# Kernel tuning notes

Hardware: AMD Instinct MI355X
Metric: run time of the kernel (lower is better)

The kernel has to match this reference:

```python
import jax, jax.numpy as jnp
import numpy as np

B, S, D, H = 2, 2048, 1024, 16
DH = D // H  # 64


def setup_inputs() -> dict:
    key = jax.random.key(0)
    ks = jax.random.split(key, 9)
    def rn(k, shape, scale=1.0):
        return jax.random.normal(k, shape, dtype=jnp.float32) * scale
    w_scale = 1.0 / np.sqrt(D)
    return {
        "queries": rn(ks[0], (B, S, D)),
        "keys": rn(ks[1], (B, S, D)),
        "values": rn(ks[2], (B, S, D)),
        "Wq": rn(ks[3], (D, D), w_scale),
        "bq": rn(ks[4], (D,), w_scale),
        "Wk": rn(ks[5], (D, D), w_scale),
        "bk": rn(ks[6], (D,), w_scale),
        "Wv": rn(ks[7], (D, D), w_scale),
        "bv": rn(ks[8], (D,), w_scale),
    }


def _split_heads(x):
    # torch: cat(split(x, DH, dim=-1), dim=0) -> index (h*B + b); equivalent to
    # [B,S,H,DH] -> [H,B,S,DH]
    bsz, slen, _ = x.shape
    return x.reshape(bsz, slen, H, DH).transpose(2, 0, 1, 3)


def reference(queries, keys, values, Wq, bq, Wk, bk, Wv, bv):
    # Linear projections (W stored so that y = x @ W + b)
    Q = queries @ Wq + bq
    K = keys @ Wk + bk
    V = values @ Wv + bv

    Qh = _split_heads(Q)  # [H,B,S,DH]
    Kh = _split_heads(K)
    Vh = _split_heads(V)

    scale = 1.0 / jnp.sqrt(jnp.asarray(DH, dtype=Qh.dtype))
    scores = jnp.einsum("hbqd,hbkd->hbqk", Qh, Kh) * scale  # [H,B,S,S]
    attn = jax.nn.softmax(scores, axis=-1)  # dropout_rate=0 -> identity
    out = jnp.einsum("hbqk,hbkd->hbqd", attn, Vh)  # [H,B,S,DH]

    # torch: cat(split(out, B, dim=0), dim=2) -> [B,S,H*DH] with head h in slice h
    out = out.transpose(1, 2, 0, 3).reshape(queries.shape[0], queries.shape[1], D)
    return out + queries  # residual; NOTE: W_O is defined but unused in the original forward
```

## Files before the change

### kernel.cpp

```cpp
#include <hip/hip_runtime.h>
#include <hip/hip_bf16.h>
#include <math.h>

#define BB 2
#define SS 2048
#define DD 1024
#define HH 16
#define DHH 64
#define MM (BB * SS)

typedef float f32x4 __attribute__((ext_vector_type(4)));
typedef __bf16 bf16x8 __attribute__((ext_vector_type(8)));

#define N_QKV ((size_t)MM * DD)
#define N_W   ((size_t)DD * DD)

__device__ unsigned short g_X [3][N_QKV];
__device__ unsigned short g_Q [N_QKV];
__device__ unsigned short g_K [N_QKV];
__device__ unsigned short g_Vt[N_QKV];
__device__ unsigned short g_Wt[3][N_W];

__device__ __forceinline__ unsigned short f2bu(float f) {
    unsigned u = __float_as_uint(f);
    unsigned r = u + 0x7FFFu + ((u >> 16) & 1u);
    return (unsigned short)(r >> 16);
}

union FragU { uint4 u; bf16x8 v; unsigned short s[8]; };
static __device__ __forceinline__ bf16x8 ldfrag(const unsigned short* p) {
    FragU f; f.u = *(const uint4*)p; return f.v;
}

__global__ __launch_bounds__(256) void cvt3(
        const float* __restrict__ x0, const float* __restrict__ x1,
        const float* __restrict__ x2, unsigned short* __restrict__ X)
{
    const float* src = blockIdx.y == 0 ? x0 : (blockIdx.y == 1 ? x1 : x2);
    unsigned short* dst = X + (size_t)blockIdx.y * N_QKV;
    const size_t i = ((size_t)blockIdx.x * 256 + threadIdx.x) * 4;
    const float4 v = *(const float4*)(src + i);
    ushort4 s;
    s.x = f2bu(v.x); s.y = f2bu(v.y); s.z = f2bu(v.z); s.w = f2bu(v.w);
    *(ushort4*)(dst + i) = s;
}

__global__ __launch_bounds__(256) void transpose_w3(
        const float* __restrict__ W0, const float* __restrict__ W1,
        const float* __restrict__ W2, unsigned short* __restrict__ Wt3)
{
    const float* W = blockIdx.z == 0 ? W0 : (blockIdx.z == 1 ? W1 : W2);
    unsigned short* Wt = Wt3 + (size_t)blockIdx.z * N_W;
    __shared__ float Ts[64][65];
    const int t = threadIdx.x;
    const int k0 = blockIdx.y * 64, n0 = blockIdx.x * 64;
#pragma unroll
    for (int i = 0; i < 16; ++i) {
        const int f = t + 256 * i, r = f >> 6, c = f & 63;
        Ts[r][c] = W[(size_t)(k0 + r) * DD + n0 + c];
    }
    __syncthreads();
#pragma unroll
    for (int i = 0; i < 16; ++i) {
        const int f = t + 256 * i, r = f >> 6, c = f & 63;
        Wt[(size_t)(n0 + r) * DD + k0 + c] = f2bu(Ts[c][r]);
    }
}

__global__ __launch_bounds__(256) void proj3(
        const unsigned short* __restrict__ X, const unsigned short* __restrict__ Wt3,
        const float* __restrict__ bq, const float* __restrict__ bk,
        const float* __restrict__ bv,
        unsigned short* __restrict__ Qp, unsigned short* __restrict__ Kp,
        unsigned short* __restrict__ Vtp)
{
    const int z = blockIdx.z;
    const unsigned short* xb = X   + (size_t)z * N_QKV;
    const unsigned short* Wt = Wt3 + (size_t)z * N_W;
    const float* bias = z == 0 ? bq : (z == 1 ? bk : bv);
    const float scale = z == 0 ? 0.125f : 1.0f;

    __shared__ unsigned short As[128][72];
    __shared__ unsigned short Bs[128][72];
    const int t = threadIdx.x, lane = t & 63, w = t >> 6;
    const int q = lane >> 4, li = lane & 15;
    const int wm = (w >> 1) * 64, wn = (w & 1) * 64;
    const int m0 = blockIdx.y * 128, n0 = blockIdx.x * 128;
    const int rs = t >> 3, cs = (t & 7) * 8;

    f32x4 acc[4][4];
#pragma unroll
    for (int mt = 0; mt < 4; ++mt)
#pragma unroll
        for (int nt = 0; nt < 4; ++nt) acc[mt][nt] = (f32x4)0.f;

    uint4 pa0, pa1, pa2, pa3, pb0, pb1, pb2, pb3;
#define PROJ_LD(kk) \
    pa0 = *(const uint4*)(xb + (size_t)(m0 + rs      ) * DD + (kk) + cs); \
    pa1 = *(const uint4*)(xb + (size_t)(m0 + rs + 32 ) * DD + (kk) + cs); \
    pa2 = *(const uint4*)(xb + (size_t)(m0 + rs + 64 ) * DD + (kk) + cs); \
    pa3 = *(const uint4*)(xb + (size_t)(m0 + rs + 96 ) * DD + (kk) + cs); \
    pb0 = *(const uint4*)(Wt + (size_t)(n0 + rs      ) * DD + (kk) + cs); \
    pb1 = *(const uint4*)(Wt + (size_t)(n0 + rs + 32 ) * DD + (kk) + cs); \
    pb2 = *(const uint4*)(Wt + (size_t)(n0 + rs + 64 ) * DD + (kk) + cs); \
    pb3 = *(const uint4*)(Wt + (size_t)(n0 + rs + 96 ) * DD + (kk) + cs);

    PROJ_LD(0)

    for (int kk = 0; kk < DD; kk += 64) {
        *(uint4*)&As[rs     ][cs] = pa0;
        *(uint4*)&As[rs + 32][cs] = pa1;
        *(uint4*)&As[rs + 64][cs] = pa2;
        *(uint4*)&As[rs + 96][cs] = pa3;
        *(uint4*)&Bs[rs     ][cs] = pb0;
        *(uint4*)&Bs[rs + 32][cs] = pb1;
        *(uint4*)&Bs[rs + 64][cs] = pb2;
        *(uint4*)&Bs[rs + 96][cs] = pb3;
        __syncthreads();
        if (kk + 64 < DD) { PROJ_LD(kk + 64) }
#pragma unroll
        for (int ks = 0; ks < 64; ks += 32) {
            bf16x8 a[4], b[4];
#pragma unroll
            for (int mt = 0; mt < 4; ++mt) a[mt] = ldfrag(&As[wm + mt * 16 + li][ks + q * 8]);
#pragma unroll
            for (int nt = 0; nt < 4; ++nt) b[nt] = ldfrag(&Bs[wn + nt * 16 + li][ks + q * 8]);
#pragma unroll
            for (int mt = 0; mt < 4; ++mt)
#pragma unroll
                for (int nt = 0; nt < 4; ++nt)
                    acc[mt][nt] = __builtin_amdgcn_mfma_f32_16x16x32_bf16(
                        a[mt], b[nt], acc[mt][nt], 0, 0, 0);
        }
        __syncthreads();
    }
#undef PROJ_LD

    float bvv[4];
#pragma unroll
    for (int nt = 0; nt < 4; ++nt) bvv[nt] = bias[n0 + wn + nt * 16 + li];

    if (z < 2) {
        unsigned short* out = z == 0 ? Qp : Kp;
#pragma unroll
        for (int mt = 0; mt < 4; ++mt)
#pragma unroll
            for (int nt = 0; nt < 4; ++nt)
#pragma unroll
                for (int reg = 0; reg < 4; ++reg) {
                    const int m = m0 + wm + mt * 16 + q * 4 + reg;
                    out[(size_t)m * DD + n0 + wn + nt * 16 + li] =
                        f2bu((acc[mt][nt][reg] + bvv[nt]) * scale);
                }
    } else {
        const int b = m0 >> 11;
        const int h = (n0 + wn) >> 6;
#pragma unroll
        for (int mt = 0; mt < 4; ++mt)
#pragma unroll
            for (int nt = 0; nt < 4; ++nt) {
                const int s = (m0 & (SS - 1)) + wm + mt * 16 + q * 4;
                const int dh = nt * 16 + li;
                ushort4 sv;
                sv.x = f2bu(acc[mt][nt][0] + bvv[nt]);
                sv.y = f2bu(acc[mt][nt][1] + bvv[nt]);
                sv.z = f2bu(acc[mt][nt][2] + bvv[nt]);
                sv.w = f2bu(acc[mt][nt][3] + bvv[nt]);
                *(ushort4*)(Vtp + ((size_t)((b * HH + h) * DHH + dh)) * SS + s) = sv;
            }
    }
}

__global__ __launch_bounds__(256) void attn3(
        const unsigned short* __restrict__ Qg, const unsigned short* __restrict__ Kg,
        const unsigned short* __restrict__ Vtg,
        const float* __restrict__ queries, float* __restrict__ outp)
{
    __shared__ unsigned short Qs [64][72];
    __shared__ unsigned short Ks [64][72];
    __shared__ unsigned short Vts[64][72];
    __shared__ unsigned short Psb[64][72];

    const int t = threadIdx.x, lane = t & 63, w = t >> 6;
    const int q = lane >> 4, li = lane & 15;
    const int qt = blockIdx.x, h = blockIdx.y, b = blockIdx.z;
    const int rs = t >> 3, cs = (t & 7) * 8;

    *(uint4*)&Qs[rs     ][cs] =
        *(const uint4*)(Qg + (size_t)(b * SS + qt * 64 + rs) * DD + h * DHH + cs);
    *(uint4*)&Qs[rs + 32][cs] =
        *(const uint4*)(Qg + (size_t)(b * SS + qt * 64 + rs + 32) * DD + h * DHH + cs);

    uint4 pk0, pk1, pv0, pv1;
#define ATTN_LD(s0) \
    pk0 = *(const uint4*)(Kg  + (size_t)(b * SS + (s0) + rs) * DD + h * DHH + cs); \
    pk1 = *(const uint4*)(Kg  + (size_t)(b * SS + (s0) + rs + 32) * DD + h * DHH + cs); \
    pv0 = *(const uint4*)(Vtg + ((size_t)((b * HH + h) * DHH + rs)) * SS + (s0) + cs); \
    pv1 = *(const uint4*)(Vtg + ((size_t)((b * HH + h) * DHH + rs + 32)) * SS + (s0) + cs);

    ATTN_LD(0)

    FragU ones;
#pragma unroll
    for (int j = 0; j < 8; ++j) ones.s[j] = 0x3F80;

    f32x4 o[4], lacc;
#pragma unroll
    for (int nt = 0; nt < 4; ++nt) o[nt] = (f32x4)0.f;
    lacc = (f32x4)0.f;

    for (int kt = 0; kt < SS / 64; ++kt) {
        *(uint4*)&Ks [rs     ][cs] = pk0;
        *(uint4*)&Ks [rs + 32][cs] = pk1;
        *(uint4*)&Vts[rs     ][cs] = pv0;
        *(uint4*)&Vts[rs + 32][cs] = pv1;
        __syncthreads();
        if (kt + 1 < SS / 64) { ATTN_LD((kt + 1) * 64) }

        f32x4 sc[4];
#pragma unroll
        for (int nt = 0; nt < 4; ++nt) sc[nt] = (f32x4)0.f;
#pragma unroll
        for (int ks = 0; ks < 64; ks += 32) {
            const bf16x8 a = ldfrag(&Qs[w * 16 + li][ks + q * 8]);
#pragma unroll
            for (int nt = 0; nt < 4; ++nt) {
                const bf16x8 bb = ldfrag(&Ks[nt * 16 + li][ks + q * 8]);
                sc[nt] = __builtin_amdgcn_mfma_f32_16x16x32_bf16(a, bb, sc[nt], 0, 0, 0);
            }
        }

#pragma unroll
        for (int nt = 0; nt < 4; ++nt)
#pragma unroll
            for (int reg = 0; reg < 4; ++reg)
                Psb[w * 16 + q * 4 + reg][nt * 16 + li] = f2bu(__expf(sc[nt][reg]));

#pragma unroll
        for (int ks = 0; ks < 64; ks += 32) {
            const bf16x8 Pa = ldfrag(&Psb[w * 16 + li][ks + q * 8]);
#pragma unroll
            for (int nt = 0; nt < 4; ++nt) {
                const bf16x8 vb = ldfrag(&Vts[nt * 16 + li][ks + q * 8]);
                o[nt] = __builtin_amdgcn_mfma_f32_16x16x32_bf16(Pa, vb, o[nt], 0, 0, 0);
            }
            lacc = __builtin_amdgcn_mfma_f32_16x16x32_bf16(Pa, ones.v, lacc, 0, 0, 0);
        }
        __syncthreads();
    }
#undef ATTN_LD

    float inv[4];
#pragma unroll
    for (int reg = 0; reg < 4; ++reg) inv[reg] = 1.f / lacc[reg];
#pragma unroll
    for (int nt = 0; nt < 4; ++nt)
#pragma unroll
        for (int reg = 0; reg < 4; ++reg) {
            const size_t g = (size_t)(b * SS + qt * 64 + w * 16 + q * 4 + reg) * DD
                           + h * DHH + nt * 16 + li;
            outp[g] = o[nt][reg] * inv[reg] + queries[g];
        }
}

extern "C" void kernel_launch(void* const* d_in, const int* in_sizes, int n_in,
                              void* d_out, int out_size, void* d_ws, size_t ws_size,
                              hipStream_t stream) {
    const float* queries = (const float*)d_in[0];
    const float* keys    = (const float*)d_in[1];
    const float* values  = (const float*)d_in[2];
    const float* Wq      = (const float*)d_in[3];
    const float* bq      = (const float*)d_in[4];
    const float* Wk      = (const float*)d_in[5];
    const float* bk      = (const float*)d_in[6];
    const float* Wv      = (const float*)d_in[7];
    const float* bv      = (const float*)d_in[8];
    float* outp = (float*)d_out;

    const size_t need = (6 * N_QKV + 3 * N_W) * sizeof(unsigned short);
    unsigned short *Xp, *Qp, *Kp, *Vtp, *Wtp;
    if (ws_size >= need) {
        Xp  = (unsigned short*)d_ws;
        Qp  = Xp + 3 * N_QKV;
        Kp  = Qp + N_QKV;
        Vtp = Kp + N_QKV;
        Wtp = Vtp + N_QKV;
    } else {
        hipGetSymbolAddress((void**)&Xp,  HIP_SYMBOL(g_X));
        hipGetSymbolAddress((void**)&Qp,  HIP_SYMBOL(g_Q));
        hipGetSymbolAddress((void**)&Kp,  HIP_SYMBOL(g_K));
        hipGetSymbolAddress((void**)&Vtp, HIP_SYMBOL(g_Vt));
        hipGetSymbolAddress((void**)&Wtp, HIP_SYMBOL(g_Wt));
    }

    const dim3 bp(256);
    cvt3<<<dim3(MM * DD / 1024, 3), bp, 0, stream>>>(queries, keys, values, Xp);
    transpose_w3<<<dim3(16, 16, 3), bp, 0, stream>>>(Wq, Wk, Wv, Wtp);
    proj3<<<dim3(8, 32, 3), bp, 0, stream>>>(Xp, Wtp, bq, bk, bv, Qp, Kp, Vtp);
    attn3<<<dim3(SS / 64, HH, BB), bp, 0, stream>>>(Qp, Kp, Vtp, queries, outp);
}
```

Baseline: 225.5 us.

## Process 128 query rows per attention block and keep Q fragments in registers

The attention kernel now gives each block 128 query rows instead of 64, and each wave handles 32 rows, so every K/V tile loaded into shared memory is reused across twice as many queries. Q fragments are hoisted into registers once, and the Q shared buffer is then reused to stage the exp(P) values, which removes the separate P buffer. K/V fragments are loaded once per k-step and shared across both row tiles. This halves the grid to 512 blocks and raises register pressure, which could reduce occupancy.

```diff
diff --git a/kernel.cpp b/kernel.cpp
--- a/kernel.cpp
+++ b/kernel.cpp
@@ -171,25 +171,27 @@
     }
 }
 
-__global__ __launch_bounds__(256) void attn3(
+__global__ __launch_bounds__(256) void attn4(
         const unsigned short* __restrict__ Qg, const unsigned short* __restrict__ Kg,
         const unsigned short* __restrict__ Vtg,
         const float* __restrict__ queries, float* __restrict__ outp)
 {
-    __shared__ unsigned short Qs [64][72];
+    __shared__ unsigned short QP [128][72];
     __shared__ unsigned short Ks [64][72];
     __shared__ unsigned short Vts[64][72];
-    __shared__ unsigned short Psb[64][72];
 
     const int t = threadIdx.x, lane = t & 63, w = t >> 6;
     const int q = lane >> 4, li = lane & 15;
     const int qt = blockIdx.x, h = blockIdx.y, b = blockIdx.z;
     const int rs = t >> 3, cs = (t & 7) * 8;
 
-    *(uint4*)&Qs[rs     ][cs] =
-        *(const uint4*)(Qg + (size_t)(b * SS + qt * 64 + rs) * DD + h * DHH + cs);
-    *(uint4*)&Qs[rs + 32][cs] =
-        *(const uint4*)(Qg + (size_t)(b * SS + qt * 64 + rs + 32) * DD + h * DHH + cs);
+    {
+        const unsigned short* qsrc = Qg + (size_t)(b * SS + qt * 128) * DD + h * DHH + cs;
+        *(uint4*)&QP[rs      ][cs] = *(const uint4*)(qsrc + (size_t)(rs      ) * DD);
+        *(uint4*)&QP[rs + 32 ][cs] = *(const uint4*)(qsrc + (size_t)(rs + 32 ) * DD);
+        *(uint4*)&QP[rs + 64 ][cs] = *(const uint4*)(qsrc + (size_t)(rs + 64 ) * DD);
+        *(uint4*)&QP[rs + 96 ][cs] = *(const uint4*)(qsrc + (size_t)(rs + 96 ) * DD);
+    }
 
     uint4 pk0, pk1, pv0, pv1;
 #define ATTN_LD(s0) \
@@ -199,68 +201,104 @@
     pv1 = *(const uint4*)(Vtg + ((size_t)((b * HH + h) * DHH + rs + 32)) * SS + (s0) + cs);
 
     ATTN_LD(0)
+    *(uint4*)&Ks [rs     ][cs] = pk0;
+    *(uint4*)&Ks [rs + 32][cs] = pk1;
+    *(uint4*)&Vts[rs     ][cs] = pv0;
+    *(uint4*)&Vts[rs + 32][cs] = pv1;
+    __syncthreads();
+
+    bf16x8 qa[2][2];
+#pragma unroll
+    for (int mt = 0; mt < 2; ++mt)
+#pragma unroll
+        for (int ki = 0; ki < 2; ++ki)
+            qa[mt][ki] = ldfrag(&QP[w * 32 + mt * 16 + li][ki * 32 + q * 8]);
 
     FragU ones;
 #pragma unroll
     for (int j = 0; j < 8; ++j) ones.s[j] = 0x3F80;
 
-    f32x4 o[4], lacc;
-#pragma unroll
-    for (int nt = 0; nt < 4; ++nt) o[nt] = (f32x4)0.f;
-    lacc = (f32x4)0.f;
+    f32x4 o[2][4], lacc[2];
+#pragma unroll
+    for (int mt = 0; mt < 2; ++mt) {
+        lacc[mt] = (f32x4)0.f;
+#pragma unroll
+        for (int nt = 0; nt < 4; ++nt) o[mt][nt] = (f32x4)0.f;
+    }
 
     for (int kt = 0; kt < SS / 64; ++kt) {
-        *(uint4*)&Ks [rs     ][cs] = pk0;
-        *(uint4*)&Ks [rs + 32][cs] = pk1;
-        *(uint4*)&Vts[rs     ][cs] = pv0;
-        *(uint4*)&Vts[rs + 32][cs] = pv1;
-        __syncthreads();
         if (kt + 1 < SS / 64) { ATTN_LD((kt + 1) * 64) }
 
-        f32x4 sc[4];
-#pragma unroll
-        for (int nt = 0; nt < 4; ++nt) sc[nt] = (f32x4)0.f;
-#pragma unroll
-        for (int ks = 0; ks < 64; ks += 32) {
-            const bf16x8 a = ldfrag(&Qs[w * 16 + li][ks + q * 8]);
-#pragma unroll
-            for (int nt = 0; nt < 4; ++nt) {
-                const bf16x8 bb = ldfrag(&Ks[nt * 16 + li][ks + q * 8]);
-                sc[nt] = __builtin_amdgcn_mfma_f32_16x16x32_bf16(a, bb, sc[nt], 0, 0, 0);
+        f32x4 sc[2][4];
+#pragma unroll
+        for (int mt = 0; mt < 2; ++mt)
+#pragma unroll
+            for (int nt = 0; nt < 4; ++nt) sc[mt][nt] = (f32x4)0.f;
+#pragma unroll
+        for (int ki = 0; ki < 2; ++ki) {
+            bf16x8 bb[4];
+#pragma unroll
+            for (int nt = 0; nt < 4; ++nt)
+                bb[nt] = ldfrag(&Ks[nt * 16 + li][ki * 32 + q * 8]);
+#pragma unroll
+            for (int mt = 0; mt < 2; ++mt)
+#pragma unroll
+                for (int nt = 0; nt < 4; ++nt)
+                    sc[mt][nt] = __builtin_amdgcn_mfma_f32_16x16x32_bf16(
+                        qa[mt][ki], bb[nt], sc[mt][nt], 0, 0, 0);
+        }
+
+#pragma unroll
+        for (int mt = 0; mt < 2; ++mt)
+#pragma unroll
+            for (int nt = 0; nt < 4; ++nt)
+#pragma unroll
+                for (int reg = 0; reg < 4; ++reg)
+                    QP[w * 32 + mt * 16 + q * 4 + reg][nt * 16 + li] =
+                        f2bu(__expf(sc[mt][nt][reg]));
+
+#pragma unroll
+        for (int ki = 0; ki < 2; ++ki) {
+            bf16x8 vb[4];
+#pragma unroll
+            for (int nt = 0; nt < 4; ++nt)
+                vb[nt] = ldfrag(&Vts[nt * 16 + li][ki * 32 + q * 8]);
+#pragma unroll
+            for (int mt = 0; mt < 2; ++mt) {
+                const bf16x8 Pa = ldfrag(&QP[w * 32 + mt * 16 + li][ki * 32 + q * 8]);
+#pragma unroll
+                for (int nt = 0; nt < 4; ++nt)
+                    o[mt][nt] = __builtin_amdgcn_mfma_f32_16x16x32_bf16(
+                        Pa, vb[nt], o[mt][nt], 0, 0, 0);
+                lacc[mt] = __builtin_amdgcn_mfma_f32_16x16x32_bf16(
+                    Pa, ones.v, lacc[mt], 0, 0, 0);
             }
         }
-
-#pragma unroll
-        for (int nt = 0; nt < 4; ++nt)
-#pragma unroll
-            for (int reg = 0; reg < 4; ++reg)
-                Psb[w * 16 + q * 4 + reg][nt * 16 + li] = f2bu(__expf(sc[nt][reg]));
-
-#pragma unroll
-        for (int ks = 0; ks < 64; ks += 32) {
-            const bf16x8 Pa = ldfrag(&Psb[w * 16 + li][ks + q * 8]);
-#pragma unroll
-            for (int nt = 0; nt < 4; ++nt) {
-                const bf16x8 vb = ldfrag(&Vts[nt * 16 + li][ks + q * 8]);
-                o[nt] = __builtin_amdgcn_mfma_f32_16x16x32_bf16(Pa, vb, o[nt], 0, 0, 0);
-            }
-            lacc = __builtin_amdgcn_mfma_f32_16x16x32_bf16(Pa, ones.v, lacc, 0, 0, 0);
+        __syncthreads();
+        if (kt + 1 < SS / 64) {
+            *(uint4*)&Ks [rs     ][cs] = pk0;
+            *(uint4*)&Ks [rs + 32][cs] = pk1;
+            *(uint4*)&Vts[rs     ][cs] = pv0;
+            *(uint4*)&Vts[rs + 32][cs] = pv1;
         }
         __syncthreads();
     }
 #undef ATTN_LD
 
-    float inv[4];
-#pragma unroll
-    for (int reg = 0; reg < 4; ++reg) inv[reg] = 1.f / lacc[reg];
-#pragma unroll
-    for (int nt = 0; nt < 4; ++nt)
-#pragma unroll
-        for (int reg = 0; reg < 4; ++reg) {
-            const size_t g = (size_t)(b * SS + qt * 64 + w * 16 + q * 4 + reg) * DD
-                           + h * DHH + nt * 16 + li;
-            outp[g] = o[nt][reg] * inv[reg] + queries[g];
-        }
+#pragma unroll
+    for (int mt = 0; mt < 2; ++mt) {
+        float inv[4];
+#pragma unroll
+        for (int reg = 0; reg < 4; ++reg) inv[reg] = 1.f / lacc[mt][reg];
+#pragma unroll
+        for (int nt = 0; nt < 4; ++nt)
+#pragma unroll
+            for (int reg = 0; reg < 4; ++reg) {
+                const size_t g = (size_t)(b * SS + qt * 128 + w * 32 + mt * 16 + q * 4 + reg) * DD
+                               + h * DHH + nt * 16 + li;
+                outp[g] = o[mt][nt][reg] * inv[reg] + queries[g];
+            }
+    }
 }
 
 extern "C" void kernel_launch(void* const* d_in, const int* in_sizes, int n_in,
@@ -297,5 +335,5 @@
     cvt3<<<dim3(MM * DD / 1024, 3), bp, 0, stream>>>(queries, keys, values, Xp);
     transpose_w3<<<dim3(16, 16, 3), bp, 0, stream>>>(Wq, Wk, Wv, Wtp);
     proj3<<<dim3(8, 32, 3), bp, 0, stream>>>(Xp, Wtp, bq, bk, bv, Qp, Kp, Vtp);
-    attn3<<<dim3(SS / 64, HH, BB), bp, 0, stream>>>(Qp, Kp, Vtp, queries, outp);
-}
+    attn4<<<dim3(SS / 128, HH, BB), bp, 0, stream>>>(Qp, Kp, Vtp, queries, outp);
+}
```

After: 213.6 us. 1.06x faster.
